# Kernel optimization log

Measured on AMD Instinct MI355X. Metric: run time of the kernel, lower is better.

## Reference

```python
import jax, jax.numpy as jnp
import numpy as np
from functools import partial

L, B, D_IN, D_MODEL, D_OUT, D_STATE = 2048, 8, 128, 256, 32, 16
D_INNER, DT_RANK, K_CONV = 2 * D_MODEL, D_MODEL // 16, 4
LOG2PI = float(np.log(2.0 * np.pi))


def setup_inputs() -> dict:
    key = jax.random.key(0)
    ks = jax.random.split(key, 16)
    sc = 0.02
    inp = {
        "s": jax.random.normal(ks[0], (L, B, D_IN), jnp.float32),
        "a": jax.random.normal(ks[1], (L, B, D_OUT), jnp.float32),
        # embedding linear
        "W_emb": jax.random.normal(ks[2], (D_IN, D_MODEL), jnp.float32) * sc,
        "b_emb": jnp.zeros((D_MODEL,), jnp.float32),
        # mamba block params
        "norm_w": jnp.ones((D_MODEL,), jnp.float32),
        "W_in": jax.random.normal(ks[3], (D_MODEL, 2 * D_INNER), jnp.float32) * sc,
        "conv_w": jax.random.normal(ks[4], (D_INNER, 1, K_CONV), jnp.float32) * sc,
        "conv_b": jnp.zeros((D_INNER,), jnp.float32),
        "W_x": jax.random.normal(ks[5], (D_INNER, DT_RANK + 2 * D_STATE), jnp.float32) * sc,
        "W_dt": jax.random.normal(ks[6], (DT_RANK, D_INNER), jnp.float32) * sc,
        "b_dt": jnp.full((D_INNER,), -2.0, jnp.float32),  # softplus(-2) ~ small init dt
        "A_log": jnp.broadcast_to(jnp.log(jnp.arange(1, D_STATE + 1, dtype=jnp.float32)), (D_INNER, D_STATE)).copy(),
        "D": jnp.ones((D_INNER,), jnp.float32),
        "W_out": jax.random.normal(ks[7], (D_INNER, D_MODEL), jnp.float32) * sc,
        # action head + log_std
        "W_head": jax.random.normal(ks[8], (D_MODEL, D_OUT), jnp.float32) * sc,
        "b_head": jnp.zeros((D_OUT,), jnp.float32),
        "log_std": jnp.zeros((D_OUT,), jnp.float32),
    }
    return inp


def _rmsnorm(x, w, eps=1e-5):
    return x * jax.lax.rsqrt(jnp.mean(x * x, axis=-1, keepdims=True) + eps) * w


def _silu(x):
    return x * jax.nn.sigmoid(x)


def _mamba_block(x, norm_w, W_in, conv_w, conv_b, W_x, W_dt, b_dt, A_log, D, W_out):
    # x: (B, L, d_model)
    resid = x
    xn = _rmsnorm(x, norm_w)
    xz = xn @ W_in                                  # (B, L, 2*d_inner)
    xp, z = jnp.split(xz, 2, axis=-1)
    # causal depthwise conv over time
    xc = jax.lax.conv_general_dilated(
        xp.transpose(0, 2, 1), conv_w, window_strides=(1,),
        padding=[(K_CONV - 1, 0)], feature_group_count=D_INNER,
        dimension_numbers=("NCH", "OIH", "NCH"))
    xp = _silu((xc + conv_b[None, :, None]).transpose(0, 2, 1))  # (B, L, d_inner)
    # input-dependent SSM params
    x_dbl = xp @ W_x                                # (B, L, dt_rank + 2*d_state)
    dt, Bm, Cm = jnp.split(x_dbl, [DT_RANK, DT_RANK + D_STATE], axis=-1)
    dt = jax.nn.softplus(dt @ W_dt + b_dt)          # (B, L, d_inner)
    A = -jnp.exp(A_log)                             # (d_inner, d_state)

    def step(h, t):
        dt_t, B_t, C_t, x_t = t                     # (B,d_i) (B,d_s) (B,d_s) (B,d_i)
        dA = jnp.exp(dt_t[..., None] * A)           # (B, d_inner, d_state)
        dBx = (dt_t * x_t)[..., None] * B_t[:, None, :]
        h = dA * h + dBx
        y = jnp.einsum("bds,bs->bd", h, C_t)
        return h, y

    h0 = jnp.zeros((x.shape[0], D_INNER, D_STATE), x.dtype)
    tm = lambda u: jnp.moveaxis(u, 1, 0)            # time-major
    _, ys = jax.lax.scan(step, h0, (tm(dt), tm(Bm), tm(Cm), tm(xp)))
    y = jnp.moveaxis(ys, 0, 1) + xp * D             # (B, L, d_inner)
    y = y * _silu(z)
    return y @ W_out + resid


def reference(s, a, W_emb, b_emb, norm_w, W_in, conv_w, conv_b, W_x, W_dt, b_dt,
              A_log, D, W_out, W_head, b_head, log_std):
    x = s @ W_emb + b_emb                           # (L, B, d_model)
    x = x.transpose(1, 0, 2)                        # (B, L, d_model)
    x = _mamba_block(x, norm_w, W_in, conv_w, conv_b, W_x, W_dt, b_dt, A_log, D, W_out)
    x = x.transpose(1, 0, 2)                        # (L, B, d_model)
    mu = x @ W_head + b_head                        # (L, B, d_out)
    # Normal(mu, exp(log_std)).log_prob(a).sum(-1)
    z = (a - mu) * jnp.exp(-log_std)
    logp = -0.5 * z * z - log_std - 0.5 * LOG2PI
    return logp.sum(axis=-1)                        # (L, B)
```

## Files before the change

kernel.cpp:

```cpp
#include <hip/hip_runtime.h>

typedef unsigned short u16;
typedef short bf16x8 __attribute__((ext_vector_type(8)));
typedef float floatx4 __attribute__((ext_vector_type(4)));

#define LSEQ 2048
#define BB 8
#define NTOK (LSEQ*BB)
#define DMODEL 256
#define DINNER 512
#define NSEG 128
#define SEG_N 64
#define SEG_L 32

__device__ __forceinline__ float siluf(float x){ return x / (1.f + __expf(-x)); }
__device__ __forceinline__ float b2f(u16 x){ return __uint_as_float(((unsigned)x) << 16); }
__device__ __forceinline__ u16 f2b(float f){
  unsigned u = __float_as_uint(f);
  unsigned r = (u + 0x7fffu + ((u >> 16) & 1u)) >> 16;
  return (u16)r;
}

__device__ __forceinline__ void gload16(const u16* g, u16* l) {
  __builtin_amdgcn_global_load_lds(
      (const __attribute__((address_space(1))) unsigned int*)g,
      (__attribute__((address_space(3))) unsigned int*)l, 16, 0, 0);
}

__device__ __forceinline__ void compute_dA(float dt, float As0, bool uni,
    const float* __restrict__ Alog, int c, float* dA)
{
  if (uni) {
    float p = __expf(dt*As0);
    float p2 = p*p, p4 = p2*p2, p8 = p4*p4;
    dA[0]=p;      dA[1]=p2;     dA[2]=p2*p;   dA[3]=p4;
    dA[4]=p4*p;   dA[5]=p4*p2;  dA[6]=p4*p2*p;dA[7]=p8;
    dA[8]=p8*p;   dA[9]=p8*p2;  dA[10]=p8*p2*p; dA[11]=p8*p4;
    dA[12]=p8*p4*p; dA[13]=p8*p4*p2; dA[14]=p8*p4*p2*p; dA[15]=p8*p8;
  } else {
    #pragma unroll
    for (int s = 0; s < 16; ++s) dA[s] = __expf(dt * (-__expf(Alog[c*16+s])));
  }
}

__global__ __launch_bounds__(256) void prep_k(
    const float* __restrict__ Wemb, const float* __restrict__ Win,
    const float* __restrict__ Wout, const float* __restrict__ Wx,
    const float* __restrict__ Wh,
    u16* __restrict__ WTe, u16* __restrict__ WTi, u16* __restrict__ WTo,
    u16* __restrict__ WxT, u16* __restrict__ WhT)
{
  __shared__ u16 T[64*66];
  int g = blockIdx.x, tid = threadIdx.x;
  if (g < 96) {
    const float* src; u16* dst; int n0, k0, srcld, dstld;
    if (g < 64) {
      int tn = g & 15, tk = g >> 4;
      n0 = tn*64; k0 = tk*64; src = Win; dst = WTi; srcld = 1024; dstld = 256;
    } else {
      int g2 = g - 64;
      int tn = g2 & 3, tk = g2 >> 2;
      n0 = tn*64; k0 = tk*64; src = Wout; dst = WTo; srcld = 256; dstld = 512;
    }
    int rr = tid >> 6, cc = tid & 63;
    #pragma unroll
    for (int p = 0; p < 16; ++p) {
      int kr = p*4 + rr;
      T[kr*66 + cc] = f2b(src[(size_t)(k0+kr)*srcld + n0 + cc]);
    }
    __syncthreads();
    #pragma unroll
    for (int p = 0; p < 16; ++p) {
      int nr = p*4 + rr;
      dst[(size_t)(n0+nr)*dstld + k0 + cc] = T[cc*66 + nr];
    }
  } else if (g < 224) {
    int idx = (g-96)*256 + tid; int n = idx >> 7, k = idx & 127;
    WTe[idx] = f2b(Wemb[(size_t)k*256 + n]);
  } else if (g < 320) {
    int idx = (g-224)*256 + tid; int n = idx >> 9, k = idx & 511;
    WxT[idx] = f2b(Wx[(size_t)k*48 + n]);
  } else {
    int idx = (g-320)*256 + tid; int j = idx >> 8, k = idx & 255;
    WhT[idx] = f2b(Wh[(size_t)k*32 + j]);
  }
}

__global__ __launch_bounds__(256) void embnorm_k(
    const float* __restrict__ s, const u16* __restrict__ WTe,
    const float* __restrict__ bemb, const float* __restrict__ nw,
    u16* __restrict__ Xb, u16* __restrict__ XNb)
{
  __shared__ u16 SH[64*264];
  __shared__ float ssq[64*4];
  __shared__ float rr[64];
  u16* As = SH;
  u16* Bs = SH + 64*40;
  const int tid = threadIdx.x;
  const int wave = tid >> 6, lane = tid & 63;
  const int quad = lane >> 4, l16 = lane & 15;
  const int m0 = blockIdx.x*64;
  const int wn = wave*64;
  const int srow = tid >> 2, sch = (tid & 3)*8;
  floatx4 acc[4][4];
  #pragma unroll
  for (int r = 0; r < 4; ++r)
    #pragma unroll
    for (int c = 0; c < 4; ++c) acc[r][c] = (floatx4){0.f,0.f,0.f,0.f};

  for (int k0 = 0; k0 < 128; k0 += 32) {
    {
      float4 v0 = *(const float4*)&s[(size_t)(m0+srow)*128 + k0 + sch];
      float4 v1 = *(const float4*)&s[(size_t)(m0+srow)*128 + k0 + sch + 4];
      __align__(16) u16 o[8];
      o[0]=f2b(v0.x); o[1]=f2b(v0.y); o[2]=f2b(v0.z); o[3]=f2b(v0.w);
      o[4]=f2b(v1.x); o[5]=f2b(v1.y); o[6]=f2b(v1.z); o[7]=f2b(v1.w);
      *(uint4*)&As[srow*40 + sch] = *(const uint4*)o;
    }
    #pragma unroll
    for (int p = 0; p < 4; ++p) {
      int row = srow + p*64;
      *(uint4*)&Bs[row*40 + sch] = *(const uint4*)&WTe[(size_t)row*128 + k0 + sch];
    }
    __syncthreads();
    bf16x8 af[4], bf[4];
    #pragma unroll
    for (int r = 0; r < 4; ++r) af[r] = *(const bf16x8*)&As[(r*16 + l16)*40 + quad*8];
    #pragma unroll
    for (int c = 0; c < 4; ++c) bf[c] = *(const bf16x8*)&Bs[(wn + c*16 + l16)*40 + quad*8];
    #pragma unroll
    for (int r = 0; r < 4; ++r)
      #pragma unroll
      for (int c = 0; c < 4; ++c)
        acc[r][c] = __builtin_amdgcn_mfma_f32_16x16x32_bf16(af[r], bf[c], acc[r][c], 0, 0, 0);
    __syncthreads();
  }
  u16* Xs = SH;
  #pragma unroll
  for (int c = 0; c < 4; ++c) {
    int n = wn + c*16 + l16;
    float bv = bemb[n];
    #pragma unroll
    for (int r = 0; r < 4; ++r)
      #pragma unroll
      for (int reg = 0; reg < 4; ++reg) {
        int ml = r*16 + quad*4 + reg;
        Xs[ml*264 + n] = f2b(acc[r][c][reg] + bv);
      }
  }
  __syncthreads();
  #pragma unroll
  for (int p = 0; p < 8; ++p) {
    int row = p*8 + (tid >> 5);
    int col = (tid & 31)*8;
    *(uint4*)&Xb[(size_t)(m0+row)*256 + col] = *(const uint4*)&Xs[row*264 + col];
  }
  const int tk = tid >> 2, q = tid & 3;
  float ss = 0.f;
  #pragma unroll
  for (int j = 0; j < 8; ++j) {
    uint4 v = *(const uint4*)&Xs[tk*264 + q*64 + j*8];
    const u16* u = (const u16*)&v;
    #pragma unroll
    for (int i = 0; i < 8; ++i) { float x = b2f(u[i]); ss += x*x; }
  }
  ssq[tk*4 + q] = ss;
  __syncthreads();
  if (q == 0)
    rr[tk] = rsqrtf((ssq[tk*4]+ssq[tk*4+1]+ssq[tk*4+2]+ssq[tk*4+3])*(1.f/DMODEL) + 1e-5f);
  __syncthreads();
  float r = rr[tk];
  #pragma unroll
  for (int j = 0; j < 8; ++j) {
    int idx = q*64 + j*8;
    uint4 v = *(const uint4*)&Xs[tk*264 + idx];
    const u16* u = (const u16*)&v;
    float4 w0 = *(const float4*)&nw[idx];
    float4 w1 = *(const float4*)&nw[idx+4];
    __align__(16) u16 o[8];
    o[0]=f2b(b2f(u[0])*r*w0.x); o[1]=f2b(b2f(u[1])*r*w0.y);
    o[2]=f2b(b2f(u[2])*r*w0.z); o[3]=f2b(b2f(u[3])*r*w0.w);
    o[4]=f2b(b2f(u[4])*r*w1.x); o[5]=f2b(b2f(u[5])*r*w1.y);
    o[6]=f2b(b2f(u[6])*r*w1.z); o[7]=f2b(b2f(u[7])*r*w1.w);
    *(uint4*)&XNb[(size_t)(m0+tk)*256 + idx] = *(const uint4*)o;
  }
}

template<int K>
__global__ __launch_bounds__(256) void gemm_mfma(
    const u16* __restrict__ Ab, const u16* __restrict__ WT,
    u16* __restrict__ Cv, int N)
{
  __shared__ __align__(16) u16 SH[17408];
  u16* As = SH;
  u16* Bs = SH + 128*64;
  const int tid = threadIdx.x;
  const int wave = tid >> 6, lane = tid & 63;
  const int quad = lane >> 4, l16 = lane & 15;
  const int bm0 = blockIdx.x*128, bn0 = blockIdx.y*128;
  const int wm = (wave & 1)*64, wn = (wave >> 1)*64;
  floatx4 acc[4][4];
  #pragma unroll
  for (int r = 0; r < 4; ++r)
    #pragma unroll
    for (int c = 0; c < 4; ++c) acc[r][c] = (floatx4){0.f,0.f,0.f,0.f};

  for (int k0 = 0; k0 < K; k0 += 64) {
    #pragma unroll
    for (int p = 0; p < 4; ++p) {
      int cid = (wave*4 + p)*64 + lane;
      int row = cid >> 3, sch = (cid & 7) ^ (row & 7);
      gload16(&Ab[(size_t)(bm0+row)*K + k0 + sch*8], As + (wave*4+p)*512);
      gload16(&WT[(size_t)(bn0+row)*K + k0 + sch*8], Bs + (wave*4+p)*512);
    }
    __syncthreads();
    #pragma unroll
    for (int ks = 0; ks < 2; ++ks) {
      bf16x8 af[4], bf[4];
      #pragma unroll
      for (int r = 0; r < 4; ++r) {
        int row = wm + r*16 + l16;
        int lch = (ks*4 + quad) ^ (row & 7);
        af[r] = *(const bf16x8*)&As[row*64 + lch*8];
      }
      #pragma unroll
      for (int c = 0; c < 4; ++c) {
        int row = wn + c*16 + l16;
        int lch = (ks*4 + quad) ^ (row & 7);
        bf[c] = *(const bf16x8*)&Bs[row*64 + lch*8];
      }
      #pragma unroll
      for (int r = 0; r < 4; ++r)
        #pragma unroll
        for (int c = 0; c < 4; ++c)
          acc[r][c] = __builtin_amdgcn_mfma_f32_16x16x32_bf16(af[r], bf[c], acc[r][c], 0, 0, 0);
    }
    __syncthreads();
  }
  u16* Cs = SH;
  #pragma unroll
  for (int c = 0; c < 4; ++c) {
    int nl = wn + c*16 + l16;
    #pragma unroll
    for (int r = 0; r < 4; ++r)
      #pragma unroll
      for (int reg = 0; reg < 4; ++reg) {
        int ml = wm + r*16 + quad*4 + reg;
        Cs[ml*136 + nl] = f2b(acc[r][c][reg]);
      }
  }
  __syncthreads();
  #pragma unroll
  for (int p = 0; p < 8; ++p) {
    int row = p*16 + (tid >> 4);
    int col = (tid & 15)*8;
    uint4 v = *(const uint4*)&Cs[row*136 + col];
    *(uint4*)&Cv[(size_t)(bm0+row)*N + bn0 + col] = v;
  }
}

__global__ __launch_bounds__(256) void xdblBC_k(const u16* __restrict__ XZb,
    const float* __restrict__ cw, const float* __restrict__ cb,
    const u16* __restrict__ WxT,
    float* __restrict__ BM, float* __restrict__ CM, float* __restrict__ DTR,
    u16* __restrict__ XPb)
{
  __shared__ u16 As[64*40];
  __shared__ u16 Ws[48*40];
  __shared__ float CWs[512*4];
  __shared__ float CBs[512];
  const int tid = threadIdx.x;
  const int wave = tid >> 6, lane = tid & 63;
  const int quad = lane >> 4, l16 = lane & 15;
  const int m0 = blockIdx.x*64;
  const int srow = tid >> 2, sch = (tid & 3)*8;
  const int n = m0 + srow;
  for (int e = tid; e < 2048; e += 256) CWs[e] = cw[e];
  for (int e = tid; e < 512;  e += 256) CBs[e] = cb[e];
  floatx4 acc[3];
  #pragma unroll
  for (int j = 0; j < 3; ++j) acc[j] = (floatx4){0.f,0.f,0.f,0.f};
  __syncthreads();
  const bf16x8 z8 = {0,0,0,0,0,0,0,0};
  for (int k0 = 0; k0 < DINNER; k0 += 32) {
    bf16x8 t3 = *(const bf16x8*)&XZb[(size_t)n*1024 + k0 + sch];
    bf16x8 t2 = z8, t1 = z8, t0v = z8;
    if (n >= 8)  t2  = *(const bf16x8*)&XZb[(size_t)(n-8)*1024  + k0 + sch];
    if (n >= 16) t1  = *(const bf16x8*)&XZb[(size_t)(n-16)*1024 + k0 + sch];
    if (n >= 24) t0v = *(const bf16x8*)&XZb[(size_t)(n-24)*1024 + k0 + sch];
    __align__(16) u16 outa[8];
    #pragma unroll
    for (int j = 0; j < 8; ++j) {
      int c = k0 + sch + j;
      float4 wv = *(const float4*)&CWs[c*4];
      float xc = CBs[c] + wv.x*b2f((u16)t0v[j]) + wv.y*b2f((u16)t1[j])
               + wv.z*b2f((u16)t2[j]) + wv.w*b2f((u16)t3[j]);
      outa[j] = f2b(siluf(xc));
    }
    *(uint4*)&As[srow*40 + sch] = *(const uint4*)outa;
    *(uint4*)&XPb[(size_t)n*DINNER + k0 + sch] = *(const uint4*)outa;
    if (tid < 192) {
      int wr = tid >> 2;
      *(uint4*)&Ws[wr*40 + sch] = *(const uint4*)&WxT[(size_t)wr*512 + k0 + sch];
    }
    __syncthreads();
    bf16x8 af = *(const bf16x8*)&As[(wave*16 + l16)*40 + quad*8];
    #pragma unroll
    for (int j = 0; j < 3; ++j) {
      bf16x8 bf = *(const bf16x8*)&Ws[(j*16 + l16)*40 + quad*8];
      acc[j] = __builtin_amdgcn_mfma_f32_16x16x32_bf16(af, bf, acc[j], 0, 0, 0);
    }
    __syncthreads();
  }
  const int tok0 = m0 + wave*16;
  #pragma unroll
  for (int reg = 0; reg < 4; ++reg) {
    size_t t = (size_t)(tok0 + quad*4 + reg);
    BM[t*16 + l16]  = acc[1][reg];
    CM[t*16 + l16]  = acc[2][reg];
    DTR[t*16 + l16] = acc[0][reg];
  }
}

__global__ __launch_bounds__(256) void scanA_k(const float* __restrict__ DTR,
    const u16* __restrict__ XPb, const float* __restrict__ BM,
    const float* __restrict__ Wdt, const float* __restrict__ bdt,
    const float* __restrict__ Alog, u16* __restrict__ HENDb,
    float* __restrict__ DTS, unsigned* __restrict__ DXb)
{
  __shared__ float ROWa[SEG_L*16];
  __shared__ float ROWb[SEG_L*16];
  const int tid = threadIdx.x;
  const int seg = blockIdx.x, b = blockIdx.y, half = blockIdx.z;
  const int c = half*256 + tid;
  const int t0 = seg*SEG_L;
  const size_t base = (size_t)t0*BB + b;
  for (int idx = tid; idx < SEG_L*16; idx += 256) {
    int t = idx >> 4, j = idx & 15;
    size_t off = (base + (size_t)t*BB)*16 + j;
    ROWa[idx] = BM[off];
    ROWb[idx] = DTR[off];
  }
  float As0 = -__expf(Alog[c*16]);
  bool uni = true;
  #pragma unroll
  for (int s = 1; s < 16; ++s) {
    float Av = -__expf(Alog[c*16+s]);
    uni = uni && (fabsf(Av - As0*(float)(s+1)) <= 1e-4f*(float)(s+1));
  }
  float wdt[16];
  #pragma unroll
  for (int r = 0; r < 16; ++r) wdt[r] = Wdt[r*DINNER + c];
  const float bd = bdt[c];
  float h[16];
  #pragma unroll
  for (int s = 0; s < 16; ++s) h[s] = 0.f;
  float dts = 0.f;
  const u16* xpp = XPb + base*DINNER + c;
  __syncthreads();
  for (int t = 0; t < SEG_L; ++t) {
    float xp = b2f(xpp[(size_t)t*BB*DINNER]);
    float dsum = bd;
    #pragma unroll
    for (int r = 0; r < 16; ++r) dsum = fmaf(ROWb[t*16+r], wdt[r], dsum);
    float dt = (dsum > 20.f) ? dsum : __logf(1.f + __expf(dsum));
    dts += dt;
    DXb[(((size_t)(t0+t)*BB + b)*DINNER + c)] = ((unsigned)f2b(xp) << 16) | f2b(dt);
    float dtx = dt * xp;
    float dA[16];
    compute_dA(dt, As0, uni, Alog, c, dA);
    float4 r0 = *(const float4*)&ROWa[t*16 + 0];
    float4 r1 = *(const float4*)&ROWa[t*16 + 4];
    float4 r2 = *(const float4*)&ROWa[t*16 + 8];
    float4 r3 = *(const float4*)&ROWa[t*16 + 12];
    h[0]  = fmaf(dA[0],  h[0],  dtx*r0.x);
    h[1]  = fmaf(dA[1],  h[1],  dtx*r0.y);
    h[2]  = fmaf(dA[2],  h[2],  dtx*r0.z);
    h[3]  = fmaf(dA[3],  h[3],  dtx*r0.w);
    h[4]  = fmaf(dA[4],  h[4],  dtx*r1.x);
    h[5]  = fmaf(dA[5],  h[5],  dtx*r1.y);
    h[6]  = fmaf(dA[6],  h[6],  dtx*r1.z);
    h[7]  = fmaf(dA[7],  h[7],  dtx*r1.w);
    h[8]  = fmaf(dA[8],  h[8],  dtx*r2.x);
    h[9]  = fmaf(dA[9],  h[9],  dtx*r2.y);
    h[10] = fmaf(dA[10], h[10], dtx*r2.z);
    h[11] = fmaf(dA[11], h[11], dtx*r2.w);
    h[12] = fmaf(dA[12], h[12], dtx*r3.x);
    h[13] = fmaf(dA[13], h[13], dtx*r3.y);
    h[14] = fmaf(dA[14], h[14], dtx*r3.z);
    h[15] = fmaf(dA[15], h[15], dtx*r3.w);
  }
  u16* hp = &HENDb[(((size_t)seg*BB + b)*DINNER + c)*16];
  #pragma unroll
  for (int q = 0; q < 2; ++q) {
    ushort4 v0, v1;
    v0.x = f2b(h[q*8+0]); v0.y = f2b(h[q*8+1]); v0.z = f2b(h[q*8+2]); v0.w = f2b(h[q*8+3]);
    v1.x = f2b(h[q*8+4]); v1.y = f2b(h[q*8+5]); v1.z = f2b(h[q*8+6]); v1.w = f2b(h[q*8+7]);
    *(ushort4*)&hp[q*8]     = v0;
    *(ushort4*)&hp[q*8 + 4] = v1;
  }
  DTS[((size_t)seg*BB + b)*DINNER + c] = dts;
}

__global__ __launch_bounds__(256) void scanC_k(const unsigned* __restrict__ DXb,
    const u16* __restrict__ XZb, const float* __restrict__ BM, const float* __restrict__ CM,
    const float* __restrict__ Alog, const float* __restrict__ Dp,
    const u16* __restrict__ HENDb, const float* __restrict__ DTS,
    u16* __restrict__ YGb)
{
  __shared__ float ROWa[SEG_L*16];
  __shared__ float ROWc[SEG_L*16];
  const int tid = threadIdx.x;
  const int seg = blockIdx.x, b = blockIdx.y, half = blockIdx.z;
  const int c = half*256 + tid;
  const int t0 = seg*SEG_L;
  const size_t base = (size_t)t0*BB + b;
  for (int idx = tid; idx < SEG_L*16; idx += 256) {
    int t = idx >> 4, j = idx & 15;
    size_t off = (base + (size_t)t*BB)*16 + j;
    ROWa[idx] = BM[off];
    ROWc[idx] = CM[off];
  }
  float As0 = -__expf(Alog[c*16]);
  bool uni = true;
  #pragma unroll
  for (int s = 1; s < 16; ++s) {
    float Av = -__expf(Alog[c*16+s]);
    uni = uni && (fabsf(Av - As0*(float)(s+1)) <= 1e-4f*(float)(s+1));
  }
  float h[16];
  #pragma unroll
  for (int s = 0; s < 16; ++s) h[s] = 0.f;
  for (int k = 0; k < seg; ++k) {
    float ds = DTS[((size_t)k*BB + b)*DINNER + c];
    const u16* hp = &HENDb[(((size_t)k*BB + b)*DINNER + c)*16];
    ushort4 a0 = *(const ushort4*)&hp[0];
    ushort4 a1 = *(const ushort4*)&hp[4];
    ushort4 a2 = *(const ushort4*)&hp[8];
    ushort4 a3 = *(const ushort4*)&hp[12];
    float dA[16];
    compute_dA(ds, As0, uni, Alog, c, dA);
    h[0]  = fmaf(h[0],  dA[0],  b2f(a0.x));
    h[1]  = fmaf(h[1],  dA[1],  b2f(a0.y));
    h[2]  = fmaf(h[2],  dA[2],  b2f(a0.z));
    h[3]  = fmaf(h[3],  dA[3],  b2f(a0.w));
    h[4]  = fmaf(h[4],  dA[4],  b2f(a1.x));
    h[5]  = fmaf(h[5],  dA[5],  b2f(a1.y));
    h[6]  = fmaf(h[6],  dA[6],  b2f(a1.z));
    h[7]  = fmaf(h[7],  dA[7],  b2f(a1.w));
    h[8]  = fmaf(h[8],  dA[8],  b2f(a2.x));
    h[9]  = fmaf(h[9],  dA[9],  b2f(a2.y));
    h[10] = fmaf(h[10], dA[10], b2f(a2.z));
    h[11] = fmaf(h[11], dA[11], b2f(a2.w));
    h[12] = fmaf(h[12], dA[12], b2f(a3.x));
    h[13] = fmaf(h[13], dA[13], b2f(a3.y));
    h[14] = fmaf(h[14], dA[14], b2f(a3.z));
    h[15] = fmaf(h[15], dA[15], b2f(a3.w));
  }
  const float Dv = Dp[c];
  const unsigned* dxp = DXb + base*DINNER + c;
  const u16* zp  = XZb + base*1024 + DINNER + c;
  u16*       ygp = YGb + base*DINNER + c;
  __syncthreads();
  for (int t = 0; t < SEG_L; ++t) {
    unsigned dx = dxp[(size_t)t*BB*DINNER];
    float zg = b2f(zp[(size_t)t*BB*1024]);
    float dt = __uint_as_float(dx << 16);
    float xp = __uint_as_float(dx & 0xffff0000u);
    float dtx = dt * xp;
    float dA[16];
    compute_dA(dt, As0, uni, Alog, c, dA);
    float4 ra0 = *(const float4*)&ROWa[t*16 + 0];
    float4 ra1 = *(const float4*)&ROWa[t*16 + 4];
    float4 ra2 = *(const float4*)&ROWa[t*16 + 8];
    float4 ra3 = *(const float4*)&ROWa[t*16 + 12];
    float4 rc0 = *(const float4*)&ROWc[t*16 + 0];
    float4 rc1 = *(const float4*)&ROWc[t*16 + 4];
    float4 rc2 = *(const float4*)&ROWc[t*16 + 8];
    float4 rc3 = *(const float4*)&ROWc[t*16 + 12];
    float y0 = 0.f, y1 = 0.f, y2 = 0.f, y3 = 0.f;
    h[0]  = fmaf(dA[0],  h[0],  dtx*ra0.x); y0 = fmaf(h[0],  rc0.x, y0);
    h[1]  = fmaf(dA[1],  h[1],  dtx*ra0.y); y1 = fmaf(h[1],  rc0.y, y1);
    h[2]  = fmaf(dA[2],  h[2],  dtx*ra0.z); y2 = fmaf(h[2],  rc0.z, y2);
    h[3]  = fmaf(dA[3],  h[3],  dtx*ra0.w); y3 = fmaf(h[3],  rc0.w, y3);
    h[4]  = fmaf(dA[4],  h[4],  dtx*ra1.x); y0 = fmaf(h[4],  rc1.x, y0);
    h[5]  = fmaf(dA[5],  h[5],  dtx*ra1.y); y1 = fmaf(h[5],  rc1.y, y1);
    h[6]  = fmaf(dA[6],  h[6],  dtx*ra1.z); y2 = fmaf(h[6],  rc1.z, y2);
    h[7]  = fmaf(dA[7],  h[7],  dtx*ra1.w); y3 = fmaf(h[7],  rc1.w, y3);
    h[8]  = fmaf(dA[8],  h[8],  dtx*ra2.x); y0 = fmaf(h[8],  rc2.x, y0);
    h[9]  = fmaf(dA[9],  h[9],  dtx*ra2.y); y1 = fmaf(h[9],  rc2.y, y1);
    h[10] = fmaf(dA[10], h[10], dtx*ra2.z); y2 = fmaf(h[10], rc2.z, y2);
    h[11] = fmaf(dA[11], h[11], dtx*ra2.w); y3 = fmaf(h[11], rc2.w, y3);
    h[12] = fmaf(dA[12], h[12], dtx*ra3.x); y0 = fmaf(h[12], rc3.x, y0);
    h[13] = fmaf(dA[13], h[13], dtx*ra3.y); y1 = fmaf(h[13], rc3.y, y1);
    h[14] = fmaf(dA[14], h[14], dtx*ra3.z); y2 = fmaf(h[14], rc3.z, y2);
    h[15] = fmaf(dA[15], h[15], dtx*ra3.w); y3 = fmaf(h[15], rc3.w, y3);
    float y = (y0+y1) + (y2+y3);
    ygp[(size_t)t*BB*DINNER] = f2b((y + xp*Dv) * siluf(zg));
  }
}

__global__ __launch_bounds__(256) void outhead_k(const u16* __restrict__ YGb,
    const u16* __restrict__ WTo, const u16* __restrict__ Xb,
    const u16* __restrict__ WhT, const float* __restrict__ bh,
    const float* __restrict__ lstd, const float* __restrict__ a,
    float* __restrict__ out)
{
  __shared__ u16 SH[(64+256)*72];
  u16* As = SH;
  u16* Bs = SH + 64*72;
  const int tid = threadIdx.x;
  const int wave = tid >> 6, lane = tid & 63;
  const int quad = lane >> 4, l16 = lane & 15;
  const int m0 = blockIdx.x*64;
  const int n0 = wave*64;
  const int srow = tid >> 3, sch = (tid & 7)*8;
  floatx4 acc[4][4];
  #pragma unroll
  for (int r = 0; r < 4; ++r)
    #pragma unroll
    for (int c = 0; c < 4; ++c) acc[r][c] = (floatx4){0.f,0.f,0.f,0.f};

  for (int k0 = 0; k0 < DINNER; k0 += 64) {
    #pragma unroll
    for (int p = 0; p < 2; ++p) {
      int row = srow + p*32;
      *(uint4*)&As[row*72 + sch] = *(const uint4*)&YGb[(size_t)(m0+row)*DINNER + k0 + sch];
    }
    #pragma unroll
    for (int p = 0; p < 8; ++p) {
      int row = srow + p*32;
      *(uint4*)&Bs[row*72 + sch] = *(const uint4*)&WTo[(size_t)row*DINNER + k0 + sch];
    }
    __syncthreads();
    #pragma unroll
    for (int ks = 0; ks < 2; ++ks) {
      bf16x8 af[4], bf[4];
      #pragma unroll
      for (int r = 0; r < 4; ++r)
        af[r] = *(const bf16x8*)&As[(r*16 + l16)*72 + ks*32 + quad*8];
      #pragma unroll
      for (int c = 0; c < 4; ++c)
        bf[c] = *(const bf16x8*)&Bs[(n0 + c*16 + l16)*72 + ks*32 + quad*8];
      #pragma unroll
      for (int r = 0; r < 4; ++r)
        #pragma unroll
        for (int c = 0; c < 4; ++c)
          acc[r][c] = __builtin_amdgcn_mfma_f32_16x16x32_bf16(af[r], bf[c], acc[r][c], 0, 0, 0);
    }
    __syncthreads();
  }
  u16* Xs = SH;
  #pragma unroll
  for (int p = 0; p < 8; ++p) {
    int row = p*8 + (tid >> 5);
    int col = (tid & 31)*8;
    *(uint4*)&Xs[row*264 + col] = *(const uint4*)&Xb[(size_t)(m0+row)*256 + col];
  }
  __syncthreads();
  #pragma unroll
  for (int c = 0; c < 4; ++c) {
    int n = n0 + c*16 + l16;
    #pragma unroll
    for (int r = 0; r < 4; ++r) {
      #pragma unroll
      for (int reg = 0; reg < 4; ++reg) {
        int ml = r*16 + quad*4 + reg;
        Xs[ml*264 + n] = f2b(acc[r][c][reg] + b2f(Xs[ml*264 + n]));
      }
    }
  }
  __syncthreads();
  floatx4 mu[2];
  mu[0] = (floatx4){0.f,0.f,0.f,0.f};
  mu[1] = (floatx4){0.f,0.f,0.f,0.f};
  #pragma unroll
  for (int k0 = 0; k0 < DMODEL; k0 += 32) {
    bf16x8 axf = *(const bf16x8*)&Xs[(wave*16 + l16)*264 + k0 + quad*8];
    #pragma unroll
    for (int nt = 0; nt < 2; ++nt) {
      bf16x8 bwf = *(const bf16x8*)(WhT + (size_t)(nt*16 + l16)*DMODEL + k0 + quad*8);
      mu[nt] = __builtin_amdgcn_mfma_f32_16x16x32_bf16(axf, bwf, mu[nt], 0, 0, 0);
    }
  }
  float ls0 = lstd[l16],      els0 = __expf(-ls0), bh0 = bh[l16];
  float ls1 = lstd[16 + l16], els1 = __expf(-ls1), bh1 = bh[16 + l16];
  #pragma unroll
  for (int reg = 0; reg < 4; ++reg) {
    int tok = m0 + wave*16 + quad*4 + reg;
    float m0v = mu[0][reg] + bh0;
    float m1v = mu[1][reg] + bh1;
    float z0 = (a[(size_t)tok*32 + l16]      - m0v) * els0;
    float z1 = (a[(size_t)tok*32 + 16 + l16] - m1v) * els1;
    float t = (-0.5f*z0*z0 - ls0) + (-0.5f*z1*z1 - ls1) - 2.f*0.91893853320467274f;
    t += __shfl_xor(t, 1);
    t += __shfl_xor(t, 2);
    t += __shfl_xor(t, 4);
    t += __shfl_xor(t, 8);
    if (l16 == 0) out[tok] = t;
  }
}

extern "C" void kernel_launch(void* const* d_in, const int* in_sizes, int n_in,
                              void* d_out, int out_size, void* d_ws, size_t ws_size,
                              hipStream_t stream)
{
  const float* s    = (const float*)d_in[0];
  const float* a    = (const float*)d_in[1];
  const float* Wemb = (const float*)d_in[2];
  const float* bemb = (const float*)d_in[3];
  const float* nw   = (const float*)d_in[4];
  const float* Win  = (const float*)d_in[5];
  const float* cw   = (const float*)d_in[6];
  const float* cb   = (const float*)d_in[7];
  const float* Wx   = (const float*)d_in[8];
  const float* Wdt  = (const float*)d_in[9];
  const float* bdt  = (const float*)d_in[10];
  const float* Alog = (const float*)d_in[11];
  const float* Dp   = (const float*)d_in[12];
  const float* Wout = (const float*)d_in[13];
  const float* Wh   = (const float*)d_in[14];
  const float* bh   = (const float*)d_in[15];
  const float* lstd = (const float*)d_in[16];

  u16*   Xb   = (u16*)d_ws;
  u16*   XZb  = Xb  + (size_t)NTOK*DMODEL;
  u16*   XNb  = XZb + (size_t)NTOK*1024;
  u16*   YGb  = XNb + (size_t)NTOK*DMODEL;
  u16*   WTe  = YGb + (size_t)NTOK*DINNER;
  u16*   WTi  = WTe + 256*128;
  u16*   WTo  = WTi + 1024*256;
  u16*   WxT  = WTo + 256*512;
  u16*   WhT  = WxT + 48*512;
  u16*   HENDb= WhT + 32*256;
  u16*   XPb  = HENDb + (size_t)NSEG*BB*DINNER*16;
  unsigned* DXb = (unsigned*)(XPb + (size_t)NTOK*DINNER);
  float* BM   = (float*)(DXb + (size_t)NTOK*DINNER);
  float* CM   = BM + (size_t)NTOK*16;
  float* DTR  = CM + (size_t)NTOK*16;
  float* DTS  = DTR + (size_t)NTOK*16;
  float* out  = (float*)d_out;

  prep_k        <<<352,         256, 0, stream>>>(Wemb, Win, Wout, Wx, Wh,
                                                  WTe, WTi, WTo, WxT, WhT);
  embnorm_k     <<<256,         256, 0, stream>>>(s, WTe, bemb, nw, Xb, XNb);
  gemm_mfma<256><<<dim3(128,8), 256, 0, stream>>>(XNb, WTi, XZb, 1024);
  xdblBC_k      <<<256,         256, 0, stream>>>(XZb, cw, cb, WxT, BM, CM, DTR, XPb);
  scanA_k       <<<dim3(SEG_N,BB,2), 256, 0, stream>>>(DTR, XPb, BM, Wdt, bdt,
                                                       Alog, HENDb, DTS, DXb);
  scanC_k       <<<dim3(SEG_N,BB,2), 256, 0, stream>>>(DXb, XZb, BM, CM,
                                                       Alog, Dp, HENDb, DTS, YGb);
  outhead_k     <<<256,         256, 0, stream>>>(YGb, WTo, Xb, WhT, bh, lstd, a, out);
}
```

Before: 245.8 us.

## Halve scan segment count, prefetch next-step loads, reverse segment block order

Segments become twice as long (32 segments of 64 steps instead of 64 of 32), which halves the serial cross-segment prefix work in the output scan but lengthens each block's sequential loop and cuts the number of parallel blocks. Both scan kernels now software-prefetch the next timestep's global loads (xp, dx, z, and the next segment's end state and dt-sum) one iteration ahead to hide memory latency. Block order in the output scan is reversed so the segments with the longest prefix loop start first. The risk is lower occupancy and parallelism from fewer segments and higher register pressure from the prefetched values.

```diff
diff --git a/kernel.cpp b/kernel.cpp
--- a/kernel.cpp
+++ b/kernel.cpp
@@ -10,8 +10,8 @@
 #define DMODEL 256
 #define DINNER 512
 #define NSEG 128
-#define SEG_N 64
-#define SEG_L 32
+#define SEG_N 32
+#define SEG_L 64
 
 __device__ __forceinline__ float siluf(float x){ return x / (1.f + __expf(-x)); }
 __device__ __forceinline__ float b2f(u16 x){ return __uint_as_float(((unsigned)x) << 16); }
@@ -358,8 +358,9 @@
   float dts = 0.f;
   const u16* xpp = XPb + base*DINNER + c;
   __syncthreads();
+  float xp = b2f(xpp[0]);
   for (int t = 0; t < SEG_L; ++t) {
-    float xp = b2f(xpp[(size_t)t*BB*DINNER]);
+    float xpn = (t+1 < SEG_L) ? b2f(xpp[(size_t)(t+1)*BB*DINNER]) : 0.f;
     float dsum = bd;
     #pragma unroll
     for (int r = 0; r < 16; ++r) dsum = fmaf(ROWb[t*16+r], wdt[r], dsum);
@@ -389,6 +390,7 @@
     h[13] = fmaf(dA[13], h[13], dtx*r3.y);
     h[14] = fmaf(dA[14], h[14], dtx*r3.z);
     h[15] = fmaf(dA[15], h[15], dtx*r3.w);
+    xp = xpn;
   }
   u16* hp = &HENDb[(((size_t)seg*BB + b)*DINNER + c)*16];
   #pragma unroll
@@ -411,7 +413,8 @@
   __shared__ float ROWa[SEG_L*16];
   __shared__ float ROWc[SEG_L*16];
   const int tid = threadIdx.x;
-  const int seg = blockIdx.x, b = blockIdx.y, half = blockIdx.z;
+  const int seg = (SEG_N - 1) - blockIdx.x;
+  const int b = blockIdx.y, half = blockIdx.z;
   const int c = half*256 + tid;
   const int t0 = seg*SEG_L;
   const size_t base = (size_t)t0*BB + b;
@@ -431,40 +434,58 @@
   float h[16];
   #pragma unroll
   for (int s = 0; s < 16; ++s) h[s] = 0.f;
-  for (int k = 0; k < seg; ++k) {
-    float ds = DTS[((size_t)k*BB + b)*DINNER + c];
-    const u16* hp = &HENDb[(((size_t)k*BB + b)*DINNER + c)*16];
-    ushort4 a0 = *(const ushort4*)&hp[0];
-    ushort4 a1 = *(const ushort4*)&hp[4];
-    ushort4 a2 = *(const ushort4*)&hp[8];
-    ushort4 a3 = *(const ushort4*)&hp[12];
-    float dA[16];
-    compute_dA(ds, As0, uni, Alog, c, dA);
-    h[0]  = fmaf(h[0],  dA[0],  b2f(a0.x));
-    h[1]  = fmaf(h[1],  dA[1],  b2f(a0.y));
-    h[2]  = fmaf(h[2],  dA[2],  b2f(a0.z));
-    h[3]  = fmaf(h[3],  dA[3],  b2f(a0.w));
-    h[4]  = fmaf(h[4],  dA[4],  b2f(a1.x));
-    h[5]  = fmaf(h[5],  dA[5],  b2f(a1.y));
-    h[6]  = fmaf(h[6],  dA[6],  b2f(a1.z));
-    h[7]  = fmaf(h[7],  dA[7],  b2f(a1.w));
-    h[8]  = fmaf(h[8],  dA[8],  b2f(a2.x));
-    h[9]  = fmaf(h[9],  dA[9],  b2f(a2.y));
-    h[10] = fmaf(h[10], dA[10], b2f(a2.z));
-    h[11] = fmaf(h[11], dA[11], b2f(a2.w));
-    h[12] = fmaf(h[12], dA[12], b2f(a3.x));
-    h[13] = fmaf(h[13], dA[13], b2f(a3.y));
-    h[14] = fmaf(h[14], dA[14], b2f(a3.z));
-    h[15] = fmaf(h[15], dA[15], b2f(a3.w));
+  if (seg > 0) {
+    float ds = DTS[((size_t)0*BB + b)*DINNER + c];
+    const u16* hp0 = &HENDb[(((size_t)0*BB + b)*DINNER + c)*16];
+    ushort4 a0 = *(const ushort4*)&hp0[0];
+    ushort4 a1 = *(const ushort4*)&hp0[4];
+    ushort4 a2 = *(const ushort4*)&hp0[8];
+    ushort4 a3 = *(const ushort4*)&hp0[12];
+    for (int k = 0; k < seg; ++k) {
+      float dsn = 0.f;
+      ushort4 n0, n1, n2, n3;
+      if (k+1 < seg) {
+        dsn = DTS[((size_t)(k+1)*BB + b)*DINNER + c];
+        const u16* hpn = &HENDb[(((size_t)(k+1)*BB + b)*DINNER + c)*16];
+        n0 = *(const ushort4*)&hpn[0];
+        n1 = *(const ushort4*)&hpn[4];
+        n2 = *(const ushort4*)&hpn[8];
+        n3 = *(const ushort4*)&hpn[12];
+      }
+      float dA[16];
+      compute_dA(ds, As0, uni, Alog, c, dA);
+      h[0]  = fmaf(h[0],  dA[0],  b2f(a0.x));
+      h[1]  = fmaf(h[1],  dA[1],  b2f(a0.y));
+      h[2]  = fmaf(h[2],  dA[2],  b2f(a0.z));
+      h[3]  = fmaf(h[3],  dA[3],  b2f(a0.w));
+      h[4]  = fmaf(h[4],  dA[4],  b2f(a1.x));
+      h[5]  = fmaf(h[5],  dA[5],  b2f(a1.y));
+      h[6]  = fmaf(h[6],  dA[6],  b2f(a1.z));
+      h[7]  = fmaf(h[7],  dA[7],  b2f(a1.w));
+      h[8]  = fmaf(h[8],  dA[8],  b2f(a2.x));
+      h[9]  = fmaf(h[9],  dA[9],  b2f(a2.y));
+      h[10] = fmaf(h[10], dA[10], b2f(a2.z));
+      h[11] = fmaf(h[11], dA[11], b2f(a2.w));
+      h[12] = fmaf(h[12], dA[12], b2f(a3.x));
+      h[13] = fmaf(h[13], dA[13], b2f(a3.y));
+      h[14] = fmaf(h[14], dA[14], b2f(a3.z));
+      h[15] = fmaf(h[15], dA[15], b2f(a3.w));
+      ds = dsn; a0 = n0; a1 = n1; a2 = n2; a3 = n3;
+    }
   }
   const float Dv = Dp[c];
   const unsigned* dxp = DXb + base*DINNER + c;
   const u16* zp  = XZb + base*1024 + DINNER + c;
   u16*       ygp = YGb + base*DINNER + c;
   __syncthreads();
+  unsigned dx = dxp[0];
+  float zg = b2f(zp[0]);
   for (int t = 0; t < SEG_L; ++t) {
-    unsigned dx = dxp[(size_t)t*BB*DINNER];
-    float zg = b2f(zp[(size_t)t*BB*1024]);
+    unsigned dxn = 0; float zgn = 0.f;
+    if (t+1 < SEG_L) {
+      dxn = dxp[(size_t)(t+1)*BB*DINNER];
+      zgn = b2f(zp[(size_t)(t+1)*BB*1024]);
+    }
     float dt = __uint_as_float(dx << 16);
     float xp = __uint_as_float(dx & 0xffff0000u);
     float dtx = dt * xp;
@@ -497,6 +518,7 @@
     h[15] = fmaf(dA[15], h[15], dtx*ra3.w); y3 = fmaf(h[15], rc3.w, y3);
     float y = (y0+y1) + (y2+y3);
     ygp[(size_t)t*BB*DINNER] = f2b((y + xp*Dv) * siluf(zg));
+    dx = dxn; zg = zgn;
   }
 }
 
```

After: 241.2 us. Within noise of the previous version (-1.9%).

## Add stitch kernel for segment-prefix states; prefetch next-step inputs in scans

Applied to the files above, without the earlier changes.

A new stitch_k kernel runs a sequential scan over the 64 segment end-states for each (batch, channel, state) triple. It overwrites HENDb in place with each segment's incoming state, so scanC_k loads its initial h directly instead of re-reducing all previous segments. That per-block reduction was quadratic in the number of segments. Both scan kernels now software-prefetch the next timestep's xp, dt and z loads to hide global latency. The change adds one kernel launch and a serial 64-step loop per thread, and the stored initial states are rounded to bf16 after accumulation.

```diff
diff --git a/kernel.cpp b/kernel.cpp
--- a/kernel.cpp
+++ b/kernel.cpp
@@ -358,8 +358,9 @@
   float dts = 0.f;
   const u16* xpp = XPb + base*DINNER + c;
   __syncthreads();
+  float xp = b2f(xpp[0]);
   for (int t = 0; t < SEG_L; ++t) {
-    float xp = b2f(xpp[(size_t)t*BB*DINNER]);
+    float xpn = (t+1 < SEG_L) ? b2f(xpp[(size_t)(t+1)*BB*DINNER]) : 0.f;
     float dsum = bd;
     #pragma unroll
     for (int r = 0; r < 16; ++r) dsum = fmaf(ROWb[t*16+r], wdt[r], dsum);
@@ -389,6 +390,7 @@
     h[13] = fmaf(dA[13], h[13], dtx*r3.y);
     h[14] = fmaf(dA[14], h[14], dtx*r3.z);
     h[15] = fmaf(dA[15], h[15], dtx*r3.w);
+    xp = xpn;
   }
   u16* hp = &HENDb[(((size_t)seg*BB + b)*DINNER + c)*16];
   #pragma unroll
@@ -402,11 +404,36 @@
   DTS[((size_t)seg*BB + b)*DINNER + c] = dts;
 }
 
+__global__ __launch_bounds__(256) void stitch_k(u16* __restrict__ HENDb,
+    const float* __restrict__ DTS, const float* __restrict__ Alog)
+{
+  int g = blockIdx.x*256 + threadIdx.x;
+  int b = g >> 13;
+  int rem = g & 8191;
+  int cidx = rem >> 4;
+  float A = -__expf(Alog[rem]);
+  float h0 = 0.f;
+  for (int k = 0; k < SEG_N; k += 4) {
+    float he[4], ds[4];
+    #pragma unroll
+    for (int u = 0; u < 4; ++u) {
+      size_t idx = (((size_t)(k+u)*BB + b) << 13) + rem;
+      he[u] = b2f(HENDb[idx]);
+      ds[u] = DTS[((size_t)(k+u)*BB + b)*DINNER + cidx];
+    }
+    #pragma unroll
+    for (int u = 0; u < 4; ++u) {
+      size_t idx = (((size_t)(k+u)*BB + b) << 13) + rem;
+      HENDb[idx] = f2b(h0);
+      h0 = fmaf(__expf(ds[u]*A), h0, he[u]);
+    }
+  }
+}
+
 __global__ __launch_bounds__(256) void scanC_k(const unsigned* __restrict__ DXb,
     const u16* __restrict__ XZb, const float* __restrict__ BM, const float* __restrict__ CM,
     const float* __restrict__ Alog, const float* __restrict__ Dp,
-    const u16* __restrict__ HENDb, const float* __restrict__ DTS,
-    u16* __restrict__ YGb)
+    const u16* __restrict__ H0b, u16* __restrict__ YGb)
 {
   __shared__ float ROWa[SEG_L*16];
   __shared__ float ROWc[SEG_L*16];
@@ -429,42 +456,25 @@
     uni = uni && (fabsf(Av - As0*(float)(s+1)) <= 1e-4f*(float)(s+1));
   }
   float h[16];
-  #pragma unroll
-  for (int s = 0; s < 16; ++s) h[s] = 0.f;
-  for (int k = 0; k < seg; ++k) {
-    float ds = DTS[((size_t)k*BB + b)*DINNER + c];
-    const u16* hp = &HENDb[(((size_t)k*BB + b)*DINNER + c)*16];
-    ushort4 a0 = *(const ushort4*)&hp[0];
-    ushort4 a1 = *(const ushort4*)&hp[4];
-    ushort4 a2 = *(const ushort4*)&hp[8];
-    ushort4 a3 = *(const ushort4*)&hp[12];
-    float dA[16];
-    compute_dA(ds, As0, uni, Alog, c, dA);
-    h[0]  = fmaf(h[0],  dA[0],  b2f(a0.x));
-    h[1]  = fmaf(h[1],  dA[1],  b2f(a0.y));
-    h[2]  = fmaf(h[2],  dA[2],  b2f(a0.z));
-    h[3]  = fmaf(h[3],  dA[3],  b2f(a0.w));
-    h[4]  = fmaf(h[4],  dA[4],  b2f(a1.x));
-    h[5]  = fmaf(h[5],  dA[5],  b2f(a1.y));
-    h[6]  = fmaf(h[6],  dA[6],  b2f(a1.z));
-    h[7]  = fmaf(h[7],  dA[7],  b2f(a1.w));
-    h[8]  = fmaf(h[8],  dA[8],  b2f(a2.x));
-    h[9]  = fmaf(h[9],  dA[9],  b2f(a2.y));
-    h[10] = fmaf(h[10], dA[10], b2f(a2.z));
-    h[11] = fmaf(h[11], dA[11], b2f(a2.w));
-    h[12] = fmaf(h[12], dA[12], b2f(a3.x));
-    h[13] = fmaf(h[13], dA[13], b2f(a3.y));
-    h[14] = fmaf(h[14], dA[14], b2f(a3.z));
-    h[15] = fmaf(h[15], dA[15], b2f(a3.w));
+  const u16* hp = &H0b[(((size_t)seg*BB + b)*DINNER + c)*16];
+  #pragma unroll
+  for (int q = 0; q < 4; ++q) {
+    ushort4 hv = *(const ushort4*)&hp[q*4];
+    h[q*4+0]=b2f(hv.x); h[q*4+1]=b2f(hv.y); h[q*4+2]=b2f(hv.z); h[q*4+3]=b2f(hv.w);
   }
   const float Dv = Dp[c];
   const unsigned* dxp = DXb + base*DINNER + c;
   const u16* zp  = XZb + base*1024 + DINNER + c;
   u16*       ygp = YGb + base*DINNER + c;
   __syncthreads();
+  unsigned dx = dxp[0];
+  float zg = b2f(zp[0]);
   for (int t = 0; t < SEG_L; ++t) {
-    unsigned dx = dxp[(size_t)t*BB*DINNER];
-    float zg = b2f(zp[(size_t)t*BB*1024]);
+    unsigned dxn = 0; float zgn = 0.f;
+    if (t+1 < SEG_L) {
+      dxn = dxp[(size_t)(t+1)*BB*DINNER];
+      zgn = b2f(zp[(size_t)(t+1)*BB*1024]);
+    }
     float dt = __uint_as_float(dx << 16);
     float xp = __uint_as_float(dx & 0xffff0000u);
     float dtx = dt * xp;
@@ -497,6 +507,7 @@
     h[15] = fmaf(dA[15], h[15], dtx*ra3.w); y3 = fmaf(h[15], rc3.w, y3);
     float y = (y0+y1) + (y2+y3);
     ygp[(size_t)t*BB*DINNER] = f2b((y + xp*Dv) * siluf(zg));
+    dx = dxn; zg = zgn;
   }
 }
 
@@ -648,7 +659,8 @@
   xdblBC_k      <<<256,         256, 0, stream>>>(XZb, cw, cb, WxT, BM, CM, DTR, XPb);
   scanA_k       <<<dim3(SEG_N,BB,2), 256, 0, stream>>>(DTR, XPb, BM, Wdt, bdt,
                                                        Alog, HENDb, DTS, DXb);
+  stitch_k      <<<256,         256, 0, stream>>>(HENDb, DTS, Alog);
   scanC_k       <<<dim3(SEG_N,BB,2), 256, 0, stream>>>(DXb, XZb, BM, CM,
-                                                       Alog, Dp, HENDb, DTS, YGb);
+                                                       Alog, Dp, HENDb, YGb);
   outhead_k     <<<256,         256, 0, stream>>>(YGb, WTo, Xb, WhT, bh, lstd, a, out);
 }
```

Measured after the change: 224.9 us. -8.5%, faster.
